# Kernel tuning notes

Hardware: AMD Instinct MI355X
Metric: run time of the kernel (lower is better)

The kernel has to match this reference:

```python
import jax, jax.numpy as jnp
import numpy as np

STRIDES = (8, 16, 32)
H = W = 640
SCORE_T = 0.5
NMS_T = 0.4


def setup_inputs() -> dict:
    key = jax.random.key(0)
    ks = jax.random.split(key, 9)
    feats = [(H // s) * (W // s) for s in STRIDES]  # 6400, 1600, 400
    d = {}
    for i, n in enumerate(feats):
        d[f"score{i}"] = jax.random.normal(ks[i], (1, n, 1), jnp.float32)
        d[f"bbox{i}"] = jax.random.normal(ks[3 + i], (1, n, 4), jnp.float32)
        d[f"kps{i}"] = jax.random.normal(ks[6 + i], (1, n, 10), jnp.float32)
    return d


def _anchors(stride):
    fh, fw = H // stride, W // stride
    yv, xv = jnp.meshgrid(jnp.arange(fh), jnp.arange(fw), indexing="ij")
    return jnp.stack([xv, yv], -1).reshape(-1, 2).astype(jnp.float32) * stride


def _decode(score, bbox, kps, stride):
    pts = _anchors(stride)                      # [N,2]
    s = jax.nn.sigmoid(score[0]).reshape(-1)    # [N]
    d = bbox[0] * stride                        # [N,4]
    x1 = pts[:, 0] - d[:, 0]
    y1 = pts[:, 1] - d[:, 1]
    x2 = pts[:, 0] + d[:, 2]
    y2 = pts[:, 1] + d[:, 3]
    b = jnp.stack([x1, y1, x2, y2], -1)         # [N,4]
    kd = (kps[0] * stride).reshape(-1, 5, 2)    # [N,5,2] (px,py pairs)
    k = (pts[:, None, :] + kd).reshape(-1, 10)  # [N,10]
    return s, b, k


def _iou(b):
    area = (b[:, 2] - b[:, 0]) * (b[:, 3] - b[:, 1])
    lt = jnp.maximum(b[:, None, :2], b[None, :, :2])
    rb = jnp.minimum(b[:, None, 2:], b[None, :, 2:])
    wh = jnp.clip(rb - lt, 0.0)
    inter = wh[..., 0] * wh[..., 1]
    return inter / (area[:, None] + area[None, :] - inter + 1e-9)


def _nms_keep(iou, valid, thresh):
    # greedy NMS on score-sorted boxes: keep i iff no earlier kept j has IoU>thresh
    n = valid.shape[0]
    def body(keep, xs):
        i, row = xs
        suppressed = jnp.any(keep & (row > thresh))
        keep = keep.at[i].set(valid[i] & ~suppressed)
        return keep, None
    keep, _ = jax.lax.scan(body, jnp.zeros(n, bool), (jnp.arange(n), iou))
    return keep


def reference(score0, score1, score2, bbox0, bbox1, bbox2, kps0, kps1, kps2):
    parts = [
        _decode(s, b, k, st)
        for s, b, k, st in zip(
            (score0, score1, score2), (bbox0, bbox1, bbox2), (kps0, kps1, kps2), STRIDES
        )
    ]
    scores = jnp.concatenate([p[0] for p in parts])  # [8400]
    boxes = jnp.concatenate([p[1] for p in parts])   # [8400,4]
    kpss = jnp.concatenate([p[2] for p in parts])    # [8400,10]
    order = jnp.argsort(-scores)                     # score-descending (NMS order)
    scores = scores[order]
    boxes = boxes[order]
    kpss = kpss[order]
    valid = scores > SCORE_T                         # threshold mask
    iou = _iou(jax.lax.stop_gradient(boxes))         # [8400,8400] ~282MB
    keep = _nms_keep(iou, valid, NMS_T)
    m = keep.astype(boxes.dtype)
    # fixed-shape equivalent of dynamic gather: suppressed rows zeroed, keep mask returned
    return boxes * m[:, None], scores * m, kpss * m[:, None], keep
```

## Files before the change

### kernel.cpp

```cpp
#include <hip/hip_runtime.h>
#include <math.h>

#define N_TOT 8400
#define MASK_WORDS 132
#define CAP 32
#define LDSN 1024
#define EC 2
#define RT 33

typedef unsigned long long u64;

__device__ __forceinline__ unsigned mono_u32(float f) {
    unsigned u = __float_as_uint(f);
    return (u & 0x80000000u) ? ~u : (u | 0x80000000u);
}

__global__ void decode_kernel(const float* __restrict__ score0, const float* __restrict__ bbox0, const float* __restrict__ kps0,
                              const float* __restrict__ score1, const float* __restrict__ bbox1, const float* __restrict__ kps1,
                              const float* __restrict__ score2, const float* __restrict__ bbox2, const float* __restrict__ kps2,
                              float* __restrict__ logit, float* __restrict__ sig,
                              float* __restrict__ box, float* __restrict__ kps,
                              u64* __restrict__ key, int* __restrict__ rank,
                              unsigned int* __restrict__ cnt,
                              u64* __restrict__ validw, u64* __restrict__ rowflag) {
    int i = blockIdx.x * blockDim.x + threadIdx.x;
    if (i >= N_TOT) return;
    if (i < MASK_WORDS) { validw[i] = 0ull; rowflag[i] = 0ull; }
    rank[i] = 0;
    cnt[i] = 0u;
    const float *sc, *bb, *kp;
    int m, F; float s;
    if (i < 6400)      { sc = score0; bb = bbox0; kp = kps0; m = i;        F = 80; s = 8.f;  }
    else if (i < 8000) { sc = score1; bb = bbox1; kp = kps1; m = i - 6400; F = 40; s = 16.f; }
    else               { sc = score2; bb = bbox2; kp = kps2; m = i - 8000; F = 20; s = 32.f; }
    float px = (float)(m % F) * s;
    float py = (float)(m / F) * s;
    float lg = sc[m];
    logit[i] = lg;
    sig[i] = 1.0f / (1.0f + expf(-lg));
    key[i] = ((u64)(~mono_u32(lg)) << 14) | (u64)i;
    float d0 = bb[m*4+0]*s, d1 = bb[m*4+1]*s, d2 = bb[m*4+2]*s, d3 = bb[m*4+3]*s;
    box[i*4+0] = px - d0;
    box[i*4+1] = py - d1;
    box[i*4+2] = px + d2;
    box[i*4+3] = py + d3;
    #pragma unroll
    for (int c = 0; c < 5; ++c) {
        kps[i*10 + 2*c]   = px + kp[m*10 + 2*c]   * s;
        kps[i*10 + 2*c+1] = py + kp[m*10 + 2*c+1] * s;
    }
}

__global__ __launch_bounds__(256) void rank_kernel(const u64* __restrict__ key, int* __restrict__ rank) {
    __shared__ u64 tile[256];
    int i = blockIdx.x * 256 + threadIdx.x;
    int t0 = blockIdx.y * 256;
    u64 ki = (i < N_TOT) ? key[i] : 0ull;
    int j = t0 + threadIdx.x;
    tile[threadIdx.x] = (j < N_TOT) ? key[j] : ~0ull;
    __syncthreads();
    if (i >= N_TOT) return;
    int rk = 0;
    #pragma unroll 8
    for (int k = 0; k < 256; ++k) {
        rk += (tile[k] < ki) ? 1 : 0;
    }
    if (rk) atomicAdd(&rank[i], rk);
}

__global__ void scatter_kernel(const int* __restrict__ rank,
                               const float* __restrict__ logit, const float* __restrict__ sig,
                               const float* __restrict__ box, const float* __restrict__ kps,
                               float* __restrict__ s_logit, float* __restrict__ s_sig,
                               float* __restrict__ s_box, float* __restrict__ s_kps,
                               u64* __restrict__ validw) {
    int i = blockIdx.x * blockDim.x + threadIdx.x;
    if (i >= N_TOT) return;
    int r = rank[i];
    float lg = logit[i];
    s_logit[r] = lg;
    s_sig[r] = sig[i];
    #pragma unroll
    for (int c = 0; c < 4; ++c)  s_box[r*4+c] = box[i*4+c];
    #pragma unroll
    for (int c = 0; c < 10; ++c) s_kps[r*10+c] = kps[i*10+c];
    if (lg > 0.f) atomicOr(&validw[r >> 6], 1ull << (r & 63));
}

__global__ __launch_bounds__(64) void pairs_kernel(const float* __restrict__ s_logit,
                                                   const float* __restrict__ s_box,
                                                   unsigned int* __restrict__ cnt,
                                                   ulonglong2* __restrict__ ent,
                                                   u64* __restrict__ rowflag) {
    int cw = blockIdx.x;
    int rb = blockIdx.y;
    if (cw < rb) return;
    int tid = threadIdx.x;

    __shared__ float cbx1[64], cby1[64], cbx2[64], cby2[64], carea[64];
    int j0 = cw * 64;
    int j = j0 + tid;
    float x1 = 0.f, y1 = 0.f, x2 = 0.f, y2 = 0.f, lgj = -1.f;
    if (j < N_TOT) {
        x1 = s_box[j*4+0]; y1 = s_box[j*4+1]; x2 = s_box[j*4+2]; y2 = s_box[j*4+3];
        lgj = s_logit[j];
    }
    cbx1[tid] = x1; cby1[tid] = y1; cbx2[tid] = x2; cby2[tid] = y2;
    carea[tid] = (x2 - x1) * (y2 - y1);
    u64 cvalid = __ballot(j < N_TOT && lgj > 0.f);
    __syncthreads();
    if (cvalid == 0ull) return;

    int r = rb * 64 + tid;
    if (r >= N_TOT) return;
    float lgr = s_logit[r];
    if (lgr <= 0.f) return;

    float rx1 = s_box[r*4+0], ry1 = s_box[r*4+1], rx2 = s_box[r*4+2], ry2 = s_box[r*4+3];
    float rarea = (rx2 - rx1) * (ry2 - ry1);
    u64 bits = 0ull;
    for (int k = 0; k < 64; ++k) {
        int jj = j0 + k;
        if (jj <= r) continue;
        if (!((cvalid >> k) & 1ull)) continue;
        float ltx = fmaxf(rx1, cbx1[k]);
        float lty = fmaxf(ry1, cby1[k]);
        float rbx = fminf(rx2, cbx2[k]);
        float rby = fminf(ry2, cby2[k]);
        float w = fmaxf(rbx - ltx, 0.f);
        float h = fmaxf(rby - lty, 0.f);
        float inter = w * h;
        float iou = inter / (rarea + carea[k] - inter + 1e-9f);
        if (iou > 0.4f) bits |= (1ull << k);
    }
    if (bits) {
        unsigned idx = atomicAdd(&cnt[r], 1u);
        if (idx < CAP) {
            ulonglong2 e; e.x = bits; e.y = (u64)cw;
            ent[(size_t)r * CAP + idx] = e;
        }
        atomicOr(&rowflag[r >> 6], 1ull << (r & 63));
    }
}

__global__ __launch_bounds__(64) void nms_kernel(const u64* __restrict__ rowflag_g,
                                                 const u64* __restrict__ validw_g,
                                                 const unsigned int* __restrict__ cnt_g,
                                                 const ulonglong2* __restrict__ ent_g,
                                                 u64* __restrict__ keep_words) {
    __shared__ unsigned short list[8448];
    __shared__ unsigned int   lcnt[LDSN];
    __shared__ ulonglong2     lent[LDSN * EC];
    int lane = threadIdx.x;

    u64 rf[3], vw[3];
    #pragma unroll
    for (int s = 0; s < 3; ++s) {
        int w = s * 64 + lane;
        rf[s] = (w < MASK_WORDS) ? rowflag_g[w] : 0ull;
        vw[s] = (w < MASK_WORDS) ? validw_g[w] : 0ull;
    }

    int base = 0;
    #pragma unroll
    for (int s = 0; s < 3; ++s) {
        int c = (int)__popcll(rf[s]);
        int x = c;
        #pragma unroll
        for (int o = 1; o < 64; o <<= 1) { int y = __shfl_up(x, o); if (lane >= o) x += y; }
        int excl = x - c;
        int total = __shfl(x, 63);
        int off = base + excl;
        u64 t = rf[s];
        int wbase = (s * 64 + lane) << 6;
        while (t) {
            int b = __builtin_ctzll(t); t &= t - 1;
            list[off++] = (unsigned short)(wbase | b);
        }
        base += total;
    }
    int n_nz = base;
    __syncthreads();

    int kcap = min(n_nz, LDSN);
    for (int k = lane; k < kcap; k += 64) {
        int r = list[k];
        unsigned c = cnt_g[r];
        lcnt[k] = c;
        unsigned cc = min(c, (unsigned)EC);
        for (unsigned e = 0; e < cc; ++e) lent[k * EC + e] = ent_g[(size_t)r * CAP + e];
    }
    __syncthreads();

    u64 rem[3] = {0ull, 0ull, 0ull};

    int r_n = 0; unsigned c_n = 0; ulonglong2 e_n; e_n.x = 0; e_n.y = 0;
    if (kcap > 0) {
        r_n = list[0];
        c_n = lcnt[0];
        if (lane < EC) e_n = lent[lane];
    }
    for (int k = 0; k < kcap; ++k) {
        int r = r_n; unsigned c = c_n; ulonglong2 ee = e_n;
        int kn = k + 1;
        if (kn < kcap) {
            r_n = list[kn];
            c_n = lcnt[kn];
            if (lane < EC) e_n = lent[kn * EC + lane];
        }
        int w = r >> 6, slot = w >> 6, owner = w & 63, b = r & 63;
        u64 remw = (slot == 0) ? rem[0] : ((slot == 1) ? rem[1] : rem[2]);
        unsigned sel = (b < 32) ? (unsigned)remw : (unsigned)(remw >> 32);
        unsigned word = (unsigned)__builtin_amdgcn_readlane((int)sel, owner);
        if (!((word >> (b & 31)) & 1u)) {
            int cc = (int)min(c, (unsigned)EC);
            for (int e = 0; e < cc; ++e) {
                unsigned ew  = (unsigned)__builtin_amdgcn_readlane((int)(unsigned)ee.y, e);
                unsigned blo = (unsigned)__builtin_amdgcn_readlane((int)(unsigned)ee.x, e);
                unsigned bhi = (unsigned)__builtin_amdgcn_readlane((int)(unsigned)(ee.x >> 32), e);
                u64 bits = ((u64)bhi << 32) | (u64)blo;
                int es = (int)(ew >> 6), eo = (int)(ew & 63u);
                u64 add = (lane == eo) ? bits : 0ull;
                if (es == 0) rem[0] |= add; else if (es == 1) rem[1] |= add; else rem[2] |= add;
            }
            if (c > (unsigned)EC) {
                unsigned cm = min(c, (unsigned)CAP);
                for (unsigned e = EC; e < cm; ++e) {
                    ulonglong2 g = ent_g[(size_t)r * CAP + e];
                    int es = (int)(g.y >> 6), eo = (int)(g.y & 63u);
                    u64 add = (lane == eo) ? g.x : 0ull;
                    if (es == 0) rem[0] |= add; else if (es == 1) rem[1] |= add; else rem[2] |= add;
                }
            }
        }
    }
    for (int k = kcap; k < n_nz; ++k) {
        int r = list[k];
        int w = r >> 6, slot = w >> 6, owner = w & 63, b = r & 63;
        u64 remw = (slot == 0) ? rem[0] : ((slot == 1) ? rem[1] : rem[2]);
        unsigned sel = (b < 32) ? (unsigned)remw : (unsigned)(remw >> 32);
        unsigned word = (unsigned)__builtin_amdgcn_readlane((int)sel, owner);
        if (!((word >> (b & 31)) & 1u)) {
            unsigned c = min(cnt_g[r], (unsigned)CAP);
            for (unsigned e = 0; e < c; ++e) {
                ulonglong2 g = ent_g[(size_t)r * CAP + e];
                int es = (int)(g.y >> 6), eo = (int)(g.y & 63u);
                u64 add = (lane == eo) ? g.x : 0ull;
                if (es == 0) rem[0] |= add; else if (es == 1) rem[1] |= add; else rem[2] |= add;
            }
        }
    }

    #pragma unroll
    for (int s = 0; s < 3; ++s) {
        int w = s * 64 + lane;
        if (w < MASK_WORDS) keep_words[w] = vw[s] & ~rem[s];
    }
}

__global__ void output_kernel(const float* __restrict__ s_sig, const float* __restrict__ s_box,
                              const float* __restrict__ s_kps,
                              const u64* __restrict__ keep_words,
                              float* __restrict__ out) {
    int r = blockIdx.x * blockDim.x + threadIdx.x;
    if (r >= N_TOT) return;
    float m = ((keep_words[r >> 6] >> (r & 63)) & 1ull) ? 1.0f : 0.0f;
    float* ob = out;
    float* os = out + 33600;
    float* okp = out + 42000;
    float* om = out + 126000;
    #pragma unroll
    for (int c = 0; c < 4; ++c)  ob[r*4+c] = s_box[r*4+c] * m;
    os[r] = s_sig[r] * m;
    #pragma unroll
    for (int c = 0; c < 10; ++c) okp[r*10+c] = s_kps[r*10+c] * m;
    om[r] = m;
}

extern "C" void kernel_launch(void* const* d_in, const int* in_sizes, int n_in,
                              void* d_out, int out_size, void* d_ws, size_t ws_size,
                              hipStream_t stream) {
    const float *score0, *bbox0, *kps0, *score1, *bbox1, *kps1, *score2, *bbox2, *kps2;
    if (in_sizes[1] == 25600) {
        score0 = (const float*)d_in[0]; bbox0 = (const float*)d_in[1]; kps0 = (const float*)d_in[2];
        score1 = (const float*)d_in[3]; bbox1 = (const float*)d_in[4]; kps1 = (const float*)d_in[5];
        score2 = (const float*)d_in[6]; bbox2 = (const float*)d_in[7]; kps2 = (const float*)d_in[8];
    } else {
        score0 = (const float*)d_in[0]; score1 = (const float*)d_in[1]; score2 = (const float*)d_in[2];
        bbox0  = (const float*)d_in[3]; bbox1  = (const float*)d_in[4]; bbox2  = (const float*)d_in[5];
        kps0   = (const float*)d_in[6]; kps1   = (const float*)d_in[7]; kps2   = (const float*)d_in[8];
    }

    char* ws = (char*)d_ws;
    float* logit   = (float*)(ws + 0);
    float* sig     = (float*)(ws + 33600);
    float* box     = (float*)(ws + 67200);
    float* kps     = (float*)(ws + 201600);
    int*   rank    = (int*)  (ws + 537600);
    float* s_logit = (float*)(ws + 571200);
    float* s_sig   = (float*)(ws + 604800);
    float* s_box   = (float*)(ws + 638400);
    float* s_kps   = (float*)(ws + 772800);
    u64*   keep_words = (u64*)(ws + 1108800);
    u64*   validw     = (u64*)(ws + 1110144);
    u64*   rowflag    = (u64*)(ws + 1111296);
    unsigned int* cnt = (unsigned int*)(ws + 1112448);
    u64*   key        = (u64*)(ws + 1146368);
    ulonglong2*   ent = (ulonglong2*)(ws + 1213568);

    float* out = (float*)d_out;

    decode_kernel<<<(N_TOT + 255) / 256, 256, 0, stream>>>(
        score0, bbox0, kps0, score1, bbox1, kps1, score2, bbox2, kps2,
        logit, sig, box, kps, key, rank, cnt, validw, rowflag);
    rank_kernel<<<dim3(RT, RT), 256, 0, stream>>>(key, rank);
    scatter_kernel<<<33, 256, 0, stream>>>(rank, logit, sig, box, kps,
                                           s_logit, s_sig, s_box, s_kps, validw);
    pairs_kernel<<<dim3(MASK_WORDS, MASK_WORDS), 64, 0, stream>>>(s_logit, s_box, cnt, ent, rowflag);
    nms_kernel<<<1, 64, 0, stream>>>(rowflag, validw, cnt, ent, keep_words);
    output_kernel<<<33, 256, 0, stream>>>(s_sig, s_box, s_kps, keep_words, out);
}
```

Before: 111.4 us.

## Register-stage NMS row entries in 32-row batches and vectorize pair IoU loop

The serial NMS kernel no longer copies counts and the first two entries per flagged row into shared memory behind a barrier. It now loads them straight into registers for batches of 32 rows, two lanes per row, prefetches the next batch, and broadcasts values with readlane. The pairs kernel reads boxes as float4, unrolls the IoU loop without data-dependent branches and applies the triangular and validity masks afterwards. This cuts LDS staging and branch divergence at the cost of some redundant IoU math. Global loads still sit on the serial critical path once per batch.

```diff
diff --git a/kernel.cpp b/kernel.cpp
--- a/kernel.cpp
+++ b/kernel.cpp
@@ -4,8 +4,6 @@
 #define N_TOT 8400
 #define MASK_WORDS 132
 #define CAP 32
-#define LDSN 1024
-#define EC 2
 #define RT 33
 
 typedef unsigned long long u64;
@@ -97,41 +95,46 @@
     if (cw < rb) return;
     int tid = threadIdx.x;
 
-    __shared__ float cbx1[64], cby1[64], cbx2[64], cby2[64], carea[64];
+    __shared__ float4 cbox[64];
+    __shared__ float  carea[64];
     int j0 = cw * 64;
     int j = j0 + tid;
-    float x1 = 0.f, y1 = 0.f, x2 = 0.f, y2 = 0.f, lgj = -1.f;
+    float4 cb = make_float4(0.f, 0.f, 0.f, 0.f);
+    float lgj = -1.f;
     if (j < N_TOT) {
-        x1 = s_box[j*4+0]; y1 = s_box[j*4+1]; x2 = s_box[j*4+2]; y2 = s_box[j*4+3];
+        cb = ((const float4*)s_box)[j];
         lgj = s_logit[j];
     }
-    cbx1[tid] = x1; cby1[tid] = y1; cbx2[tid] = x2; cby2[tid] = y2;
-    carea[tid] = (x2 - x1) * (y2 - y1);
+    cbox[tid] = cb;
+    carea[tid] = (cb.z - cb.x) * (cb.w - cb.y);
     u64 cvalid = __ballot(j < N_TOT && lgj > 0.f);
     __syncthreads();
     if (cvalid == 0ull) return;
 
     int r = rb * 64 + tid;
-    if (r >= N_TOT) return;
-    float lgr = s_logit[r];
-    if (lgr <= 0.f) return;
-
-    float rx1 = s_box[r*4+0], ry1 = s_box[r*4+1], rx2 = s_box[r*4+2], ry2 = s_box[r*4+3];
-    float rarea = (rx2 - rx1) * (ry2 - ry1);
+    float lgr = (r < N_TOT) ? s_logit[r] : -1.f;
+    if (__ballot(lgr > 0.f) == 0ull) return;
+
     u64 bits = 0ull;
-    for (int k = 0; k < 64; ++k) {
-        int jj = j0 + k;
-        if (jj <= r) continue;
-        if (!((cvalid >> k) & 1ull)) continue;
-        float ltx = fmaxf(rx1, cbx1[k]);
-        float lty = fmaxf(ry1, cby1[k]);
-        float rbx = fminf(rx2, cbx2[k]);
-        float rby = fminf(ry2, cby2[k]);
-        float w = fmaxf(rbx - ltx, 0.f);
-        float h = fmaxf(rby - lty, 0.f);
-        float inter = w * h;
-        float iou = inter / (rarea + carea[k] - inter + 1e-9f);
-        if (iou > 0.4f) bits |= (1ull << k);
+    if (lgr > 0.f) {
+        float4 rb4 = ((const float4*)s_box)[r];
+        float rarea = (rb4.z - rb4.x) * (rb4.w - rb4.y);
+        #pragma unroll 4
+        for (int k = 0; k < 64; ++k) {
+            float4 c4 = cbox[k];
+            float ltx = fmaxf(rb4.x, c4.x);
+            float lty = fmaxf(rb4.y, c4.y);
+            float rbx = fminf(rb4.z, c4.z);
+            float rby = fminf(rb4.w, c4.w);
+            float w = fmaxf(rbx - ltx, 0.f);
+            float h = fmaxf(rby - lty, 0.f);
+            float inter = w * h;
+            float iou = inter / (rarea + carea[k] - inter + 1e-9f);
+            bits |= (iou > 0.4f) ? (1ull << k) : 0ull;
+        }
+        u64 m = cvalid;
+        if (cw == rb) m &= (tid == 63) ? 0ull : (~0ull << (tid + 1));
+        bits &= m;
     }
     if (bits) {
         unsigned idx = atomicAdd(&cnt[r], 1u);
@@ -149,8 +152,6 @@
                                                  const ulonglong2* __restrict__ ent_g,
                                                  u64* __restrict__ keep_words) {
     __shared__ unsigned short list[8448];
-    __shared__ unsigned int   lcnt[LDSN];
-    __shared__ ulonglong2     lent[LDSN * EC];
     int lane = threadIdx.x;
 
     u64 rf[3], vw[3];
@@ -182,75 +183,64 @@
     int n_nz = base;
     __syncthreads();
 
-    int kcap = min(n_nz, LDSN);
-    for (int k = lane; k < kcap; k += 64) {
-        int r = list[k];
-        unsigned c = cnt_g[r];
-        lcnt[k] = c;
-        unsigned cc = min(c, (unsigned)EC);
-        for (unsigned e = 0; e < cc; ++e) lent[k * EC + e] = ent_g[(size_t)r * CAP + e];
-    }
-    __syncthreads();
-
-    u64 rem[3] = {0ull, 0ull, 0ull};
-
-    int r_n = 0; unsigned c_n = 0; ulonglong2 e_n; e_n.x = 0; e_n.y = 0;
-    if (kcap > 0) {
-        r_n = list[0];
-        c_n = lcnt[0];
-        if (lane < EC) e_n = lent[lane];
-    }
-    for (int k = 0; k < kcap; ++k) {
-        int r = r_n; unsigned c = c_n; ulonglong2 ee = e_n;
-        int kn = k + 1;
-        if (kn < kcap) {
-            r_n = list[kn];
-            c_n = lcnt[kn];
-            if (lane < EC) e_n = lent[kn * EC + lane];
-        }
-        int w = r >> 6, slot = w >> 6, owner = w & 63, b = r & 63;
-        u64 remw = (slot == 0) ? rem[0] : ((slot == 1) ? rem[1] : rem[2]);
-        unsigned sel = (b < 32) ? (unsigned)remw : (unsigned)(remw >> 32);
-        unsigned word = (unsigned)__builtin_amdgcn_readlane((int)sel, owner);
-        if (!((word >> (b & 31)) & 1u)) {
-            int cc = (int)min(c, (unsigned)EC);
-            for (int e = 0; e < cc; ++e) {
-                unsigned ew  = (unsigned)__builtin_amdgcn_readlane((int)(unsigned)ee.y, e);
-                unsigned blo = (unsigned)__builtin_amdgcn_readlane((int)(unsigned)ee.x, e);
-                unsigned bhi = (unsigned)__builtin_amdgcn_readlane((int)(unsigned)(ee.x >> 32), e);
-                u64 bits = ((u64)bhi << 32) | (u64)blo;
-                int es = (int)(ew >> 6), eo = (int)(ew & 63u);
-                u64 add = (lane == eo) ? bits : 0ull;
-                if (es == 0) rem[0] |= add; else if (es == 1) rem[1] |= add; else rem[2] |= add;
+    u64 rem0 = 0ull, rem1 = 0ull, rem2 = 0ull;
+
+    if (n_nz > 0) {
+        int half = lane >> 5;
+        int sub  = lane & 31;
+
+        int idx0 = min(sub, n_nz - 1);
+        int rowCur = list[idx0];
+        unsigned cntCur = cnt_g[rowCur];
+        ulonglong2 entCur = ent_g[(size_t)rowCur * CAP + half];
+
+        for (int k0 = 0; k0 < n_nz; k0 += 32) {
+            int nb = k0 + 32;
+            int rowNxt = 0; unsigned cntNxt = 0u;
+            ulonglong2 entNxt; entNxt.x = 0ull; entNxt.y = 0ull;
+            if (nb < n_nz) {
+                int idx = min(nb + sub, n_nz - 1);
+                rowNxt = list[idx];
+                cntNxt = cnt_g[rowNxt];
+                entNxt = ent_g[(size_t)rowNxt * CAP + half];
             }
-            if (c > (unsigned)EC) {
-                unsigned cm = min(c, (unsigned)CAP);
-                for (unsigned e = EC; e < cm; ++e) {
-                    ulonglong2 g = ent_g[(size_t)r * CAP + e];
-                    int es = (int)(g.y >> 6), eo = (int)(g.y & 63u);
-                    u64 add = (lane == eo) ? g.x : 0ull;
-                    if (es == 0) rem[0] |= add; else if (es == 1) rem[1] |= add; else rem[2] |= add;
+
+            int lim = min(32, n_nz - k0);
+            for (int i = 0; i < lim; ++i) {
+                int r = __builtin_amdgcn_readlane(rowCur, i);
+                int w = r >> 6, slot = w >> 6, owner = w & 63, b = r & 63;
+                u64 rw = (slot == 0) ? rem0 : ((slot == 1) ? rem1 : rem2);
+                unsigned halfw = (b < 32) ? (unsigned)rw : (unsigned)(rw >> 32);
+                unsigned word = (unsigned)__builtin_amdgcn_readlane((int)halfw, owner);
+                if (!((word >> (b & 31)) & 1u)) {
+                    unsigned c = (unsigned)__builtin_amdgcn_readlane((int)cntCur, i);
+                    int ec = (int)min(c, 2u);
+                    for (int e = 0; e < ec; ++e) {
+                        int src = e * 32 + i;
+                        unsigned ey  = (unsigned)__builtin_amdgcn_readlane((int)(unsigned)entCur.y, src);
+                        unsigned blo = (unsigned)__builtin_amdgcn_readlane((int)(unsigned)entCur.x, src);
+                        unsigned bhi = (unsigned)__builtin_amdgcn_readlane((int)(unsigned)(entCur.x >> 32), src);
+                        u64 bits = ((u64)bhi << 32) | (u64)blo;
+                        int es = (int)(ey >> 6), eo = (int)(ey & 63u);
+                        u64 add = (lane == eo) ? bits : 0ull;
+                        if (es == 0) rem0 |= add; else if (es == 1) rem1 |= add; else rem2 |= add;
+                    }
+                    if (c > 2u) {
+                        unsigned cm = min(c, (unsigned)CAP);
+                        for (unsigned e = 2; e < cm; ++e) {
+                            ulonglong2 g = ent_g[(size_t)r * CAP + e];
+                            int es = (int)(g.y >> 6), eo = (int)(g.y & 63u);
+                            u64 add = (lane == eo) ? g.x : 0ull;
+                            if (es == 0) rem0 |= add; else if (es == 1) rem1 |= add; else rem2 |= add;
+                        }
+                    }
                 }
             }
+            rowCur = rowNxt; cntCur = cntNxt; entCur = entNxt;
         }
     }
-    for (int k = kcap; k < n_nz; ++k) {
-        int r = list[k];
-        int w = r >> 6, slot = w >> 6, owner = w & 63, b = r & 63;
-        u64 remw = (slot == 0) ? rem[0] : ((slot == 1) ? rem[1] : rem[2]);
-        unsigned sel = (b < 32) ? (unsigned)remw : (unsigned)(remw >> 32);
-        unsigned word = (unsigned)__builtin_amdgcn_readlane((int)sel, owner);
-        if (!((word >> (b & 31)) & 1u)) {
-            unsigned c = min(cnt_g[r], (unsigned)CAP);
-            for (unsigned e = 0; e < c; ++e) {
-                ulonglong2 g = ent_g[(size_t)r * CAP + e];
-                int es = (int)(g.y >> 6), eo = (int)(g.y & 63u);
-                u64 add = (lane == eo) ? g.x : 0ull;
-                if (es == 0) rem[0] |= add; else if (es == 1) rem[1] |= add; else rem[2] |= add;
-            }
-        }
-    }
-
+
+    u64 rem[3] = {rem0, rem1, rem2};
     #pragma unroll
     for (int s = 0; s < 3; ++s) {
         int w = s * 64 + lane;
```

Result: faster. 107.9 us (-3.1%).
